# Kernel tuning notes

Hardware: AMD Instinct MI355X
Metric: run time of the kernel (lower is better)

Reference implementation:

```python
import jax, jax.numpy as jnp
import numpy as np

W_SIZE = 7
C_DIM = 256
HEADS = 8
HEAD_DIM = 32
HIDDEN = 1024
B, H, W = 32, 56, 56


def _rel_pos_index(w):
    coords = np.stack(np.meshgrid(np.arange(w), np.arange(w), indexing='ij'))  # (2,w,w)
    cf = coords.reshape(2, -1)                       # (2, w*w)
    rc = (cf[:, :, None] - cf[:, None, :]).transpose(1, 2, 0)  # (N,N,2)
    rc[:, :, 0] += w - 1
    rc[:, :, 1] += w - 1
    rc[:, :, 0] *= 2 * w - 1
    return rc.sum(-1)  # (N,N) int

REL_IDX = jnp.asarray(_rel_pos_index(W_SIZE))


def setup_inputs() -> dict:
    key = jax.random.key(0)
    ks = jax.random.split(key, 10)
    s = 0.02
    return {
        'x': jax.random.normal(ks[0], (B, H, W, C_DIM), jnp.float32),
        'norm1_g': jnp.ones((C_DIM,), jnp.float32),
        'norm1_b': jnp.zeros((C_DIM,), jnp.float32),
        'qkv_w': jax.random.normal(ks[1], (3 * C_DIM, C_DIM), jnp.float32) * s,
        'qkv_b': jnp.zeros((3 * C_DIM,), jnp.float32),
        'bias_table': jax.random.normal(ks[2], ((2 * W_SIZE - 1) ** 2, HEADS), jnp.float32) * s,
        'proj_w': jax.random.normal(ks[3], (C_DIM, C_DIM), jnp.float32) * s,
        'proj_b': jnp.zeros((C_DIM,), jnp.float32),
        'norm2_g': jnp.ones((C_DIM,), jnp.float32),
        'norm2_b': jnp.zeros((C_DIM,), jnp.float32),
        'ffn_w1': jax.random.normal(ks[4], (HIDDEN, C_DIM), jnp.float32) * s,
        'ffn_b1': jnp.zeros((HIDDEN,), jnp.float32),
        'ffn_w2': jax.random.normal(ks[5], (C_DIM, HIDDEN), jnp.float32) * s,
        'ffn_b2': jnp.zeros((C_DIM,), jnp.float32),
    }


def _ln(x, g, b, eps=1e-5):
    m = jnp.mean(x, -1, keepdims=True)
    v = jnp.mean(jnp.square(x - m), -1, keepdims=True)
    return (x - m) * jax.lax.rsqrt(v + eps) * g + b


def reference(x, norm1_g, norm1_b, qkv_w, qkv_b, bias_table, proj_w, proj_b,
              norm2_g, norm2_b, ffn_w1, ffn_b1, ffn_w2, ffn_b2):
    b, h, w, c = x.shape
    ws = W_SIZE
    n = ws * ws
    scale = HEAD_DIM ** -0.5
    shortcut = x

    y = _ln(x, norm1_g, norm1_b)
    # window partition ('block' mode): (B,H,W,C) -> (B*nW, ws*ws, C)
    y = y.reshape(b, h // ws, ws, w // ws, ws, c).transpose(0, 1, 3, 2, 4, 5)
    y = y.reshape(-1, n, c)
    bw = y.shape[0]  # num_windows * B

    qkv = y @ qkv_w.T + qkv_b                               # (bw, n, 3C)
    qkv = qkv.reshape(bw, n, 3, HEADS, HEAD_DIM).transpose(2, 0, 3, 1, 4)
    q, k, v = qkv[0] * scale, qkv[1], qkv[2]                # (bw, heads, n, d)

    attn = jnp.einsum('bhnd,bhmd->bhnm', q, k)              # (bw, heads, n, n)
    rel_bias = bias_table[REL_IDX].transpose(2, 0, 1)       # (heads, n, n)
    attn = jax.nn.softmax(attn + rel_bias[None], axis=-1)

    o = jnp.einsum('bhnm,bhmd->bhnd', attn, v)              # (bw, heads, n, d)
    o = o.transpose(0, 2, 1, 3).reshape(bw, n, c)
    o = o @ proj_w.T + proj_b

    # window reverse
    o = o.reshape(b, h // ws, w // ws, ws, ws, c).transpose(0, 1, 3, 2, 4, 5)
    o = o.reshape(b, h, w, c)

    x = shortcut + o
    z = _ln(x, norm2_g, norm2_b)
    z = jax.nn.gelu(z @ ffn_w1.T + ffn_b1, approximate=False) @ ffn_w2.T + ffn_b2
    return x + z
```

## Files before the change

### kernel.cpp

```cpp
#include <hip/hip_runtime.h>
#include <math.h>

typedef unsigned short u16;
typedef __attribute__((ext_vector_type(8))) __bf16 bf16x8;
typedef __attribute__((ext_vector_type(8))) u16 u16x8;
typedef __attribute__((ext_vector_type(4))) float f32x4;

__device__ __forceinline__ float b2f(u16 u) {
    union { unsigned int u; float f; } a; a.u = ((unsigned int)u) << 16; return a.f;
}
__device__ __forceinline__ u16 f2b(float f) {
    union { float f; unsigned int u; } a; a.f = f;
    return (u16)((a.u + 0x7fffu + ((a.u >> 16) & 1u)) >> 16);
}

__device__ __forceinline__ float gelu_t(float x) {
    float u = 1.5957691216057308f * (x + 0.044715f * x * x * x);
    float e = __expf(u);
    float t = (e - 1.0f) / (e + 1.0f);
    return 0.5f * x * (1.0f + t);
}

__device__ __forceinline__ int win2spatial(int r) {
    int wid = r / 49;
    int n   = r - wid * 49;
    int b   = wid >> 6;
    int wr  = wid & 63;
    int h   = (wr >> 3) * 7 + n / 7;
    int w   = (wr & 7) * 7 + n % 7;
    return (b * 56 + h) * 56 + w;
}

__device__ __forceinline__ void stage16(const u16* g, u16* l) {
    __builtin_amdgcn_global_load_lds((const __attribute__((address_space(1))) void*)g,
                                     (__attribute__((address_space(3))) void*)l, 16, 0, 0);
}

__global__ __launch_bounds__(256) void cvt_kernel(const float* __restrict__ in,
                                                  u16* __restrict__ out, int n)
{
    int i = (blockIdx.x * 256 + threadIdx.x) * 4;
    if (i < n) {
        float4 v = *reinterpret_cast<const float4*>(in + i);
        ushort4 o;
        o.x = f2b(v.x); o.y = f2b(v.y); o.z = f2b(v.z); o.w = f2b(v.w);
        *reinterpret_cast<ushort4*>(out + i) = o;
    }
}

__global__ __launch_bounds__(256) void bias_prep(const float* __restrict__ btab,
                                                 float* __restrict__ btile)
{
    int head = blockIdx.x;
    for (int idx = threadIdx.x; idx < 4096; idx += 256) {
        int i = idx >> 6, j = idx & 63;
        float v = -1e30f;
        if (i < 49 && j < 49) {
            int di = i / 7 - j / 7 + 6;
            int dj = i % 7 - j % 7 + 6;
            v = btab[(di * 13 + dj) * 8 + head];
        }
        btile[head * 4096 + idx] = v;
    }
}

template<int REORDER, int INBF>
__global__ __launch_bounds__(256) void ln_kernel(const void* __restrict__ inp,
                                                 const float* __restrict__ gw,
                                                 const float* __restrict__ bw,
                                                 u16* __restrict__ outp)
{
    int wave = threadIdx.x >> 6, lane = threadIdx.x & 63;
    int row  = blockIdx.x * 4 + wave;
    int irow = REORDER ? win2spatial(row) : row;

    float v[4];
    if (INBF) {
        ushort4 xx = *reinterpret_cast<const ushort4*>((const u16*)inp + (size_t)irow * 256 + lane * 4);
        v[0] = b2f(xx.x); v[1] = b2f(xx.y); v[2] = b2f(xx.z); v[3] = b2f(xx.w);
    } else {
        float4 xx = *reinterpret_cast<const float4*>((const float*)inp + (size_t)irow * 256 + lane * 4);
        v[0] = xx.x; v[1] = xx.y; v[2] = xx.z; v[3] = xx.w;
    }

    float s = v[0] + v[1] + v[2] + v[3];
    float q = v[0]*v[0] + v[1]*v[1] + v[2]*v[2] + v[3]*v[3];
#pragma unroll
    for (int off = 32; off > 0; off >>= 1) {
        s += __shfl_xor(s, off, 64);
        q += __shfl_xor(q, off, 64);
    }
    float mean = s * (1.0f / 256.0f);
    float var  = q * (1.0f / 256.0f) - mean * mean;
    float rstd = rsqrtf(var + 1e-5f);

    int c = lane * 4;
    ushort4 o;
    o.x = f2b((v[0] - mean) * rstd * gw[c + 0] + bw[c + 0]);
    o.y = f2b((v[1] - mean) * rstd * gw[c + 1] + bw[c + 1]);
    o.z = f2b((v[2] - mean) * rstd * gw[c + 2] + bw[c + 2]);
    o.w = f2b((v[3] - mean) * rstd * gw[c + 3] + bw[c + 3]);
    *reinterpret_cast<ushort4*>(outp + (size_t)row * 256 + c) = o;
}

template<int EPI>
__global__ __launch_bounds__(256) void gemm_kernel(
    const u16* __restrict__ A, const u16* __restrict__ W,
    const float* __restrict__ bias,
    u16* __restrict__ outU, float* __restrict__ outF,
    const float* __restrict__ residF, const u16* __restrict__ residU,
    int N, int K, int nB)
{
    __shared__ char smem[40960];
    u16* sA = (u16*)smem;
    u16* sB = (u16*)(smem + 16384);

    int t = threadIdx.x;
    int w = t >> 6, lane = t & 63;
    int quad = lane >> 4, l16 = lane & 15;
    int wm = (w >> 1) * 64, wn = (w & 1) * 64;

    int b = blockIdx.x;
    int xcd = b & 7, g = b >> 3;
    int n_i = g % nB;
    int m_i = (g / nB) * 8 + xcd;
    int n_blk = n_i * 128, m_blk = m_i * 128;

    int srow = t >> 3;
    int scol = ((t & 7) ^ (srow & 7)) * 8;
    const u16* pA = A + (size_t)(m_blk + srow) * K + scol;
    const u16* pB = W + (size_t)(n_blk + srow) * K + scol;
    u16* lA = sA + w * 64 * 8;
    u16* lB = sB + w * 64 * 8;

    f32x4 acc[4][4];
#pragma unroll
    for (int i = 0; i < 4; ++i)
#pragma unroll
        for (int j = 0; j < 4; ++j) acc[i][j] = (f32x4){0.f, 0.f, 0.f, 0.f};

    for (int kb = 0; kb < K; kb += 64) {
        if (kb) __syncthreads();
#pragma unroll
        for (int gg = 0; gg < 4; ++gg) {
            stage16(pA + (size_t)(gg * 32) * K + kb, lA + gg * 2048);
            stage16(pB + (size_t)(gg * 32) * K + kb, lB + gg * 2048);
        }
        __syncthreads();

#pragma unroll
        for (int q32 = 0; q32 < 2; ++q32) {
            bf16x8 af[4], bfr[4];
            int kc = q32 * 4 + quad;
#pragma unroll
            for (int tm = 0; tm < 4; ++tm) {
                int row = wm + tm * 16 + l16;
                af[tm] = *(const bf16x8*)(sA + (unsigned)(row * 8 + (kc ^ (row & 7))) * 8);
            }
#pragma unroll
            for (int tn = 0; tn < 4; ++tn) {
                int row = wn + tn * 16 + l16;
                bfr[tn] = *(const bf16x8*)(sB + (unsigned)(row * 8 + (kc ^ (row & 7))) * 8);
            }
#pragma unroll
            for (int tm = 0; tm < 4; ++tm)
#pragma unroll
                for (int tn = 0; tn < 4; ++tn)
                    acc[tm][tn] = __builtin_amdgcn_mfma_f32_16x16x32_bf16(af[tm], bfr[tn], acc[tm][tn], 0, 0, 0);
        }
    }

    if (EPI == 3) {
#pragma unroll
        for (int tn = 0; tn < 4; ++tn) {
            int col = n_blk + wn + tn * 16 + l16;
            float bv = bias[col];
#pragma unroll
            for (int tm = 0; tm < 4; ++tm)
#pragma unroll
                for (int r = 0; r < 4; ++r) {
                    int row = m_blk + wm + tm * 16 + quad * 4 + r;
                    size_t o = (size_t)row * N + col;
                    outF[o] = b2f(residU[o]) + acc[tm][tn][r] + bv;
                }
        }
        return;
    }

    __syncthreads();
    u16* tp = (u16*)smem + w * 5120;

#pragma unroll
    for (int tn = 0; tn < 4; ++tn) {
        int colL = tn * 16 + l16;
        float bv = bias[n_blk + wn + colL];
#pragma unroll
        for (int tm = 0; tm < 4; ++tm)
#pragma unroll
            for (int r = 0; r < 4; ++r) {
                int rowL = tm * 16 + quad * 4 + r;
                float val = acc[tm][tn][r] + bv;
                if (EPI == 1) val = gelu_t(val);
                if (EPI == 2) {
                    int sr = win2spatial(m_blk + wm + rowL);
                    val += residF[(size_t)sr * 256 + n_blk + wn + colL];
                }
                tp[rowL * 80 + colL] = f2b(val);
            }
    }
#pragma unroll
    for (int it = 0; it < 8; ++it) {
        int rowL = it * 8 + (lane >> 3);
        int chunk = (lane & 7) * 8;
        u16x8 vv = *(const u16x8*)(tp + rowL * 80 + chunk);
        int grow = m_blk + wm + rowL;
        if (EPI == 2) {
            *(u16x8*)(outU + (size_t)win2spatial(grow) * 256 + n_blk + wn + chunk) = vv;
        } else {
            *(u16x8*)(outU + (size_t)grow * N + n_blk + wn + chunk) = vv;
        }
    }
}

__global__ __launch_bounds__(64) void attn_kernel(const u16* __restrict__ qkv,
                                                  const float* __restrict__ btile,
                                                  u16* __restrict__ o)
{
    __shared__ u16 vT[32 * 72];
    __shared__ u16 pl[64 * 72];

    int wid = blockIdx.x, head = blockIdx.y;
    int lane = threadIdx.x;
    int quad = lane >> 4, l16 = lane & 15;

    const u16* wbase = qkv + (size_t)wid * 49 * 768;

    {
        unsigned long long* z = (unsigned long long*)vT;
        for (int i = lane; i < 576; i += 64) z[i] = 0ull;
    }

    if (lane < 49) {
#pragma unroll
        for (int c = 0; c < 4; ++c) {
            u16x8 vv = *(const u16x8*)(wbase + (size_t)lane * 768 + 512 + head * 32 + c * 8);
#pragma unroll
            for (int i = 0; i < 8; ++i) vT[(c * 8 + i) * 72 + lane] = vv[i];
        }
    }

    bf16x8 aq[4], bk[4];
#pragma unroll
    for (int t = 0; t < 4; ++t) {
        int r = t * 16 + l16; r = r > 48 ? 48 : r;
        aq[t] = *(const bf16x8*)(wbase + (size_t)r * 768 + head * 32 + quad * 8);
        bk[t] = *(const bf16x8*)(wbase + (size_t)r * 768 + 256 + head * 32 + quad * 8);
    }

    f32x4 s[4][4];
#pragma unroll
    for (int tm = 0; tm < 4; ++tm)
#pragma unroll
        for (int tn = 0; tn < 4; ++tn)
            s[tm][tn] = __builtin_amdgcn_mfma_f32_16x16x32_bf16(aq[tm], bk[tn],
                        (f32x4){0.f, 0.f, 0.f, 0.f}, 0, 0, 0);

    const float scale = 0.17677669529663687f;
    const float* bt = btile + head * 4096;
#pragma unroll
    for (int tm = 0; tm < 4; ++tm)
#pragma unroll
        for (int tn = 0; tn < 4; ++tn)
#pragma unroll
            for (int r = 0; r < 4; ++r) {
                float bb = bt[(tm * 16 + quad * 4 + r) * 64 + tn * 16 + l16];
                s[tm][tn][r] = s[tm][tn][r] * scale + bb;
            }

#pragma unroll
    for (int tm = 0; tm < 4; ++tm)
#pragma unroll
        for (int r = 0; r < 4; ++r) {
            float mx = fmaxf(fmaxf(s[tm][0][r], s[tm][1][r]), fmaxf(s[tm][2][r], s[tm][3][r]));
#pragma unroll
            for (int off = 1; off < 16; off <<= 1) mx = fmaxf(mx, __shfl_xor(mx, off, 64));
            float sum = 0.f;
#pragma unroll
            for (int tn = 0; tn < 4; ++tn) {
                float e = __expf(s[tm][tn][r] - mx);
                s[tm][tn][r] = e; sum += e;
            }
#pragma unroll
            for (int off = 1; off < 16; off <<= 1) sum += __shfl_xor(sum, off, 64);
            float inv = 1.0f / sum;
#pragma unroll
            for (int tn = 0; tn < 4; ++tn) s[tm][tn][r] *= inv;
        }

    __syncthreads();
#pragma unroll
    for (int tm = 0; tm < 4; ++tm)
#pragma unroll
        for (int tn = 0; tn < 4; ++tn)
#pragma unroll
            for (int r = 0; r < 4; ++r)
                pl[(tm * 16 + quad * 4 + r) * 72 + tn * 16 + l16] = f2b(s[tm][tn][r]);
    __syncthreads();

    f32x4 oa[4][2];
#pragma unroll
    for (int tm = 0; tm < 4; ++tm)
#pragma unroll
        for (int tn = 0; tn < 2; ++tn) oa[tm][tn] = (f32x4){0.f, 0.f, 0.f, 0.f};

#pragma unroll
    for (int ks = 0; ks < 2; ++ks) {
        bf16x8 pa[4], vb[2];
#pragma unroll
        for (int tm = 0; tm < 4; ++tm)
            pa[tm] = *(const bf16x8*)(pl + (unsigned)(tm * 16 + l16) * 72 + ks * 32 + quad * 8);
#pragma unroll
        for (int tn = 0; tn < 2; ++tn)
            vb[tn] = *(const bf16x8*)(vT + (unsigned)(tn * 16 + l16) * 72 + ks * 32 + quad * 8);
#pragma unroll
        for (int tm = 0; tm < 4; ++tm)
#pragma unroll
            for (int tn = 0; tn < 2; ++tn)
                oa[tm][tn] = __builtin_amdgcn_mfma_f32_16x16x32_bf16(pa[tm], vb[tn], oa[tm][tn], 0, 0, 0);
    }

    u16* ob = o + (size_t)wid * 49 * 256 + head * 32;
#pragma unroll
    for (int tm = 0; tm < 4; ++tm)
#pragma unroll
        for (int r = 0; r < 4; ++r) {
            int m = tm * 16 + quad * 4 + r;
            if (m < 49) {
#pragma unroll
                for (int tn = 0; tn < 2; ++tn)
                    ob[(size_t)m * 256 + tn * 16 + l16] = f2b(oa[tm][tn][r]);
            }
        }
}

extern "C" void kernel_launch(void* const* d_in, const int* in_sizes, int n_in,
                              void* d_out, int out_size, void* d_ws, size_t ws_size,
                              hipStream_t stream)
{
    const float* x     = (const float*)d_in[0];
    const float* n1g   = (const float*)d_in[1];
    const float* n1b   = (const float*)d_in[2];
    const float* qkvw  = (const float*)d_in[3];
    const float* qkvb  = (const float*)d_in[4];
    const float* btab  = (const float*)d_in[5];
    const float* projw = (const float*)d_in[6];
    const float* projb = (const float*)d_in[7];
    const float* n2g   = (const float*)d_in[8];
    const float* n2b   = (const float*)d_in[9];
    const float* w1    = (const float*)d_in[10];
    const float* b1    = (const float*)d_in[11];
    const float* w2    = (const float*)d_in[12];
    const float* b2    = (const float*)d_in[13];

    char* ws  = (char*)d_ws;
    u16* x1   = (u16*)ws;
    u16* bufA = (u16*)(ws + 102760448);
    u16* bufB = (u16*)(ws + 102760448 + 205520896);
    u16* wq   = (u16*)(ws + 102760448 + 205520896 + 51380224);
    u16* wp   = wq + 196608;
    u16* wf1  = wp + 65536;
    u16* wf2  = wf1 + 262144;
    float* btile = (float*)(ws + 102760448 + 154140672);

    cvt_kernel<<<192, 256, 0, stream>>>(qkvw, wq, 196608);
    cvt_kernel<<<64,  256, 0, stream>>>(projw, wp, 65536);
    cvt_kernel<<<256, 256, 0, stream>>>(w1, wf1, 262144);
    cvt_kernel<<<256, 256, 0, stream>>>(w2, wf2, 262144);
    bias_prep<<<8, 256, 0, stream>>>(btab, btile);

    ln_kernel<1, 0><<<25088, 256, 0, stream>>>(x, n1g, n1b, bufB);
    gemm_kernel<0><<<6 * 784, 256, 0, stream>>>(bufB, wq, qkvb, bufA, nullptr,
                                                nullptr, nullptr, 768, 256, 6);
    attn_kernel<<<dim3(2048, 8), 64, 0, stream>>>(bufA, btile, bufB);
    gemm_kernel<2><<<2 * 784, 256, 0, stream>>>(bufB, wp, projb, x1, nullptr,
                                                x, nullptr, 256, 256, 2);
    ln_kernel<0, 1><<<25088, 256, 0, stream>>>(x1, n2g, n2b, bufB);
    gemm_kernel<1><<<8 * 784, 256, 0, stream>>>(bufB, wf1, b1, bufA, nullptr,
                                                nullptr, nullptr, 1024, 256, 8);
    gemm_kernel<3><<<2 * 784, 256, 0, stream>>>(bufA, wf2, b2, nullptr, (float*)d_out,
                                                nullptr, x1, 256, 1024, 2);
}
```

Measured before the change: 691.6 us.

## Double-buffer A tile in GEMM, vectorize epilogues, use hardware bf16 convert

The GEMM main loop now double-buffers the A operand in LDS, prefetching the next K-slice while the current one is computed. It uses raw s_barrier and explicit vmcnt waits instead of full __syncthreads. The final fp32-output epilogue (EPI 3) now goes through LDS and writes vectorized float4 stores instead of scattered scalar stores, but it rounds the accumulator to bf16 before adding the residual. Also included: a cheaper tanh-GELU formula using rcp, a native bf16 conversion, and a smaller LDS transpose pitch, at the cost of a small precision loss in the final output.

New measurement: 563.7 us. 1.23x faster.

```diff
diff --git a/kernel.cpp b/kernel.cpp
--- a/kernel.cpp
+++ b/kernel.cpp
@@ -10,15 +10,14 @@
     union { unsigned int u; float f; } a; a.u = ((unsigned int)u) << 16; return a.f;
 }
 __device__ __forceinline__ u16 f2b(float f) {
-    union { float f; unsigned int u; } a; a.f = f;
-    return (u16)((a.u + 0x7fffu + ((a.u >> 16) & 1u)) >> 16);
+    union { __bf16 h; u16 u; } c; c.h = (__bf16)f; return c.u;
 }
 
 __device__ __forceinline__ float gelu_t(float x) {
-    float u = 1.5957691216057308f * (x + 0.044715f * x * x * x);
-    float e = __expf(u);
-    float t = (e - 1.0f) / (e + 1.0f);
-    return 0.5f * x * (1.0f + t);
+    float x2 = x * x;
+    float u  = x * fmaf(0.0713548162726f, x2, 1.5957691216057308f);
+    float e  = __expf(u);
+    return x * e * __builtin_amdgcn_rcpf(e + 1.0f);
 }
 
 __device__ __forceinline__ int win2spatial(int r) {
@@ -111,9 +110,10 @@
     const float* __restrict__ residF, const u16* __restrict__ residU,
     int N, int K, int nB)
 {
-    __shared__ char smem[40960];
-    u16* sA = (u16*)smem;
-    u16* sB = (u16*)(smem + 16384);
+    __shared__ char smem[49152];
+    u16* sA0 = (u16*)smem;
+    u16* sA1 = (u16*)(smem + 16384);
+    u16* sB  = (u16*)(smem + 32768);
 
     int t = threadIdx.x;
     int w = t >> 6, lane = t & 63;
@@ -130,8 +130,9 @@
     int scol = ((t & 7) ^ (srow & 7)) * 8;
     const u16* pA = A + (size_t)(m_blk + srow) * K + scol;
     const u16* pB = W + (size_t)(n_blk + srow) * K + scol;
-    u16* lA = sA + w * 64 * 8;
-    u16* lB = sB + w * 64 * 8;
+    u16* lA0 = sA0 + w * 512;
+    u16* lA1 = sA1 + w * 512;
+    u16* lB  = sB  + w * 512;
 
     f32x4 acc[4][4];
 #pragma unroll
@@ -139,15 +140,30 @@
 #pragma unroll
         for (int j = 0; j < 4; ++j) acc[i][j] = (f32x4){0.f, 0.f, 0.f, 0.f};
 
-    for (int kb = 0; kb < K; kb += 64) {
-        if (kb) __syncthreads();
-#pragma unroll
-        for (int gg = 0; gg < 4; ++gg) {
-            stage16(pA + (size_t)(gg * 32) * K + kb, lA + gg * 2048);
+    int nk = K >> 6;
+
+#pragma unroll
+    for (int gg = 0; gg < 4; ++gg)
+        stage16(pA + (size_t)(gg * 32) * K, lA0 + gg * 2048);
+
+    for (int tt = 0; tt < nk; ++tt) {
+        int kb = tt << 6;
+        __builtin_amdgcn_s_barrier();
+#pragma unroll
+        for (int gg = 0; gg < 4; ++gg)
             stage16(pB + (size_t)(gg * 32) * K + kb, lB + gg * 2048);
-        }
-        __syncthreads();
-
+        if (tt + 1 < nk) {
+            u16* lAn = (tt & 1) ? lA0 : lA1;
+#pragma unroll
+            for (int gg = 0; gg < 4; ++gg)
+                stage16(pA + (size_t)(gg * 32) * K + kb + 64, lAn + gg * 2048);
+            asm volatile("s_waitcnt vmcnt(4)" ::: "memory");
+        } else {
+            asm volatile("s_waitcnt vmcnt(0)" ::: "memory");
+        }
+        __builtin_amdgcn_s_barrier();
+
+        const u16* cA = (tt & 1) ? sA1 : sA0;
 #pragma unroll
         for (int q32 = 0; q32 < 2; ++q32) {
             bf16x8 af[4], bfr[4];
@@ -155,7 +171,7 @@
 #pragma unroll
             for (int tm = 0; tm < 4; ++tm) {
                 int row = wm + tm * 16 + l16;
-                af[tm] = *(const bf16x8*)(sA + (unsigned)(row * 8 + (kc ^ (row & 7))) * 8);
+                af[tm] = *(const bf16x8*)(cA + (unsigned)(row * 8 + (kc ^ (row & 7))) * 8);
             }
 #pragma unroll
             for (int tn = 0; tn < 4; ++tn) {
@@ -170,51 +186,47 @@
         }
     }
 
-    if (EPI == 3) {
-#pragma unroll
-        for (int tn = 0; tn < 4; ++tn) {
-            int col = n_blk + wn + tn * 16 + l16;
-            float bv = bias[col];
-#pragma unroll
-            for (int tm = 0; tm < 4; ++tm)
-#pragma unroll
-                for (int r = 0; r < 4; ++r) {
-                    int row = m_blk + wm + tm * 16 + quad * 4 + r;
-                    size_t o = (size_t)row * N + col;
-                    outF[o] = b2f(residU[o]) + acc[tm][tn][r] + bv;
-                }
-        }
-        return;
-    }
-
     __syncthreads();
-    u16* tp = (u16*)smem + w * 5120;
-
-#pragma unroll
-    for (int tn = 0; tn < 4; ++tn) {
-        int colL = tn * 16 + l16;
-        float bv = bias[n_blk + wn + colL];
-#pragma unroll
-        for (int tm = 0; tm < 4; ++tm)
-#pragma unroll
-            for (int r = 0; r < 4; ++r) {
-                int rowL = tm * 16 + quad * 4 + r;
-                float val = acc[tm][tn][r] + bv;
+    u16* tp = (u16*)smem + w * 4608;
+
+#pragma unroll
+    for (int tm = 0; tm < 4; ++tm)
+#pragma unroll
+        for (int r = 0; r < 4; ++r) {
+            int rowL = tm * 16 + quad * 4 + r;
+            int srw = 0;
+            if (EPI == 2) srw = win2spatial(m_blk + wm + rowL);
+#pragma unroll
+            for (int tn = 0; tn < 4; ++tn) {
+                int colL = tn * 16 + l16;
+                float val = acc[tm][tn][r] + bias[n_blk + wn + colL];
                 if (EPI == 1) val = gelu_t(val);
-                if (EPI == 2) {
-                    int sr = win2spatial(m_blk + wm + rowL);
-                    val += residF[(size_t)sr * 256 + n_blk + wn + colL];
-                }
-                tp[rowL * 80 + colL] = f2b(val);
-            }
-    }
+                if (EPI == 2) val += residF[(size_t)srw * 256 + n_blk + wn + colL];
+                tp[rowL * 72 + colL] = f2b(val);
+            }
+        }
+
 #pragma unroll
     for (int it = 0; it < 8; ++it) {
         int rowL = it * 8 + (lane >> 3);
         int chunk = (lane & 7) * 8;
-        u16x8 vv = *(const u16x8*)(tp + rowL * 80 + chunk);
+        u16x8 vv = *(const u16x8*)(tp + rowL * 72 + chunk);
         int grow = m_blk + wm + rowL;
-        if (EPI == 2) {
+        if (EPI == 3) {
+            size_t o = (size_t)grow * N + n_blk + wn + chunk;
+            u16x8 rr = *(const u16x8*)(residU + o);
+            float4 f0, f1;
+            f0.x = b2f(vv[0]) + b2f(rr[0]);
+            f0.y = b2f(vv[1]) + b2f(rr[1]);
+            f0.z = b2f(vv[2]) + b2f(rr[2]);
+            f0.w = b2f(vv[3]) + b2f(rr[3]);
+            f1.x = b2f(vv[4]) + b2f(rr[4]);
+            f1.y = b2f(vv[5]) + b2f(rr[5]);
+            f1.z = b2f(vv[6]) + b2f(rr[6]);
+            f1.w = b2f(vv[7]) + b2f(rr[7]);
+            *reinterpret_cast<float4*>(outF + o)     = f0;
+            *reinterpret_cast<float4*>(outF + o + 4) = f1;
+        } else if (EPI == 2) {
             *(u16x8*)(outU + (size_t)win2spatial(grow) * 256 + n_blk + wn + chunk) = vv;
         } else {
             *(u16x8*)(outU + (size_t)grow * N + n_blk + wn + chunk) = vv;
```
